# Kernel optimization log

Hardware: AMD Instinct MI355X
Metric: run time of the kernel (lower is better)

## Reference

```python
import jax, jax.numpy as jnp
import numpy as np

B, TQ, TP, D = 4, 512, 512, 256


def setup_inputs() -> dict:
    key = jax.random.key(0)
    ks = jax.random.split(key, 5)
    return {
        "q": jax.random.normal(ks[0], (B, TQ, D), dtype=jnp.float32),
        "p": jax.random.normal(ks[1], (B, TP, D), dtype=jnp.float32),
        "W0": jax.random.normal(ks[2], (D, D), dtype=jnp.float32) / np.sqrt(D),
        "W1": jax.random.normal(ks[3], (D, D), dtype=jnp.float32) / np.sqrt(D),
        "vc": jax.random.normal(ks[4], (D, 1), dtype=jnp.float32) * 0.05,
    }


def reference(q, p, W0, W1, vc):
    # q: [B,Tq,Dq], p: [B,Tp,Dp]
    prod_q = jnp.einsum('bqd,de->bqe', q, W0)   # [B,Tq,dim]
    prod_p = jnp.einsum('bpd,de->bpe', p, W1)   # [B,Tp,dim]
    # additive attention energies: tanh over broadcast sum [B,Tp,Tq,dim]
    energy = jnp.tanh(prod_p[:, :, None, :] + prod_q[:, None, :, :])
    scores = jnp.einsum('bpqe,e->bpq', energy, vc[:, 0])  # [B,Tp,Tq]
    # original softmax is over axis=-2 of [B,Tp,Tq], i.e. the Tp axis
    weights = jax.nn.softmax(scores, axis=1)   # [B,Tp,Tq]
    # weighted sum over the Tq axis of (tiled) q
    attention_q = jnp.einsum('bpq,bqd->bpd', weights, q)  # [B,Tp,Dq]
    return attention_q
```

## Files before the change

### kernel.cpp

```cpp
#include <hip/hip_runtime.h>

#define NB 4
#define TT 512
#define DD 256
#define K2L2E    2.885390081777927f
#define NEG2L2E (-2.885390081777927f)

#if defined(__has_builtin)
# if __has_builtin(__builtin_amdgcn_global_load_lds)
#  define HAS_GLL 1
# endif
#endif

typedef float v2f __attribute__((ext_vector_type(2)));

__device__ __forceinline__ v2f pk_fma(v2f a, v2f b, v2f c) {
#if defined(__has_builtin)
# if __has_builtin(__builtin_elementwise_fma)
    return __builtin_elementwise_fma(a, b, c);
# else
    v2f r; r.x = __builtin_fmaf(a.x, b.x, c.x); r.y = __builtin_fmaf(a.y, b.y, c.y); return r;
# endif
#else
    v2f r; r.x = __builtin_fmaf(a.x, b.x, c.x); r.y = __builtin_fmaf(a.y, b.y, c.y); return r;
#endif
}
__device__ __forceinline__ v2f splat2(float s) { v2f r; r.x = s; r.y = s; return r; }

__device__ __forceinline__ void stage16(const float* __restrict__ g, float* l) {
#ifdef HAS_GLL
    __builtin_amdgcn_global_load_lds((const __attribute__((address_space(1))) void*)g,
                                     (__attribute__((address_space(3))) void*)l, 16, 0, 0);
#else
    *(float4*)l = *(const float4*)g;
#endif
}

__global__ __launch_bounds__(256) void proj_exp_kernel(
    const float* __restrict__ qin, const float* __restrict__ pin,
    const float* __restrict__ W0, const float* __restrict__ W1,
    float* __restrict__ expQ, float* __restrict__ expP)
{
    const int blk = blockIdx.x;
    const int wh = blk >> 8, tid = blk & 255;
    const int m0 = (tid >> 2) * 32, n0 = (tid & 3) * 64;
    const float* A = wh ? pin : qin;
    const float* W = wh ? W1 : W0;
    float* OUT     = wh ? expP : expQ;

    __shared__ __align__(16) float As[32 * 34];
    __shared__ __align__(16) float Bs[32 * 64];

    const int t  = threadIdx.x;
    const int ar = t >> 3, ac4 = (t & 7) * 4;
    const int br = t >> 4, bc4 = (t & 15) * 4;
    const int tn = t >> 4, tm = t & 15;

    const float* Ap = A + (long)(m0 + ar) * DD + ac4;

    float4 av  = *(const float4*)Ap;
    float4 bv0 = *(const float4*)(W + (long)br * DD + n0 + bc4);
    float4 bv1 = *(const float4*)(W + (long)(br + 16) * DD + n0 + bc4);

    float acc[2][4] = {};

    for (int c = 0; c < 8; ++c) {
        As[(ac4 + 0) * 34 + ar] = av.x;
        As[(ac4 + 1) * 34 + ar] = av.y;
        As[(ac4 + 2) * 34 + ar] = av.z;
        As[(ac4 + 3) * 34 + ar] = av.w;
        *(float4*)&Bs[br * 64 + bc4]        = bv0;
        *(float4*)&Bs[(br + 16) * 64 + bc4] = bv1;
        __syncthreads();
        if (c < 7) {
            int k1 = (c + 1) * 32;
            av  = *(const float4*)(Ap + k1);
            bv0 = *(const float4*)(W + (long)(k1 + br) * DD + n0 + bc4);
            bv1 = *(const float4*)(W + (long)(k1 + 16 + br) * DD + n0 + bc4);
        }
        #pragma unroll
        for (int kk = 0; kk < 32; ++kk) {
            float2 a = *(const float2*)&As[kk * 34 + 2 * tm];
            float4 b = *(const float4*)&Bs[kk * 64 + 4 * tn];
            float aa[2] = {a.x, a.y};
            float bb[4] = {b.x, b.y, b.z, b.w};
            #pragma unroll
            for (int i = 0; i < 2; ++i)
                #pragma unroll
                for (int j = 0; j < 4; ++j)
                    acc[i][j] = __builtin_fmaf(aa[i], bb[j], acc[i][j]);
        }
        __syncthreads();
    }

    const int  bi = m0 >> 9;
    const int  ml = (m0 & 511) + 2 * tm;
    #pragma unroll
    for (int j = 0; j < 4; ++j) {
        int d = n0 + 4 * tn + j;
        float2 st;
        st.x = __builtin_amdgcn_exp2f(acc[0][j] * K2L2E);
        st.y = __builtin_amdgcn_exp2f(acc[1][j] * K2L2E);
        *(float2*)(OUT + ((long)bi * DD + d) * TT + ml) = st;
    }
}

__global__ __launch_bounds__(512, 6) void score_kernel(
    const float* __restrict__ expP, const float* __restrict__ expQ,
    const float* __restrict__ vc, float* __restrict__ ebuf, float* __restrict__ lpart)
{
    const int b = blockIdx.z, pt = blockIdx.y, qt = blockIdx.x;
    const int p0 = pt * 32, q0 = qt * 64;
    const int t  = threadIdx.x;
    const int qx = t & 31, py = t >> 5;

    __shared__ __align__(16) float PA[128 * 32];
    __shared__ __align__(16) float QB[128 * 64];
    __shared__ float vcs[DD];

    const float* gP = expP + (long)b * DD * TT + p0;
    const float* gQ = expQ + (long)b * DD * TT + q0;

    #pragma unroll
    for (int s = 0; s < 2; ++s) {
        int f = t + 512 * s, d = f >> 3, off = (f & 7) * 4;
        stage16(gP + (long)d * TT + off, &PA[f * 4]);
    }
    #pragma unroll
    for (int s = 0; s < 4; ++s) {
        int f = t + 512 * s, d = f >> 4, off = (f & 15) * 4;
        stage16(gQ + (long)d * TT + off, &QB[f * 4]);
    }
    if (t < DD) vcs[t] = vc[t];
    __syncthreads();

    v2f acc[2]; acc[0] = splat2(0.f); acc[1] = splat2(0.f);

    for (int c = 0; c < 2; ++c) {
        if (c == 1) {
            __syncthreads();
            #pragma unroll
            for (int s = 0; s < 2; ++s) {
                int f = t + 512 * s, d = f >> 3, off = (f & 7) * 4;
                stage16(gP + (long)(128 + d) * TT + off, &PA[f * 4]);
            }
            #pragma unroll
            for (int s = 0; s < 4; ++s) {
                int f = t + 512 * s, d = f >> 4, off = (f & 15) * 4;
                stage16(gQ + (long)(128 + d) * TT + off, &QB[f * 4]);
            }
            __syncthreads();
        }
        const float* vcb = &vcs[c * 128];
        #pragma unroll 8
        for (int dp = 0; dp < 64; ++dp) {
            float2 vp = *(const float2*)&vcb[2 * dp];
            v2f vsv = splat2(vp.x + vp.y);
            v2f vx  = splat2(vp.x), vy = splat2(vp.y);
            float2 A0 = *(const float2*)&PA[(2 * dp) * 32 + 2 * py];
            float2 A1 = *(const float2*)&PA[(2 * dp + 1) * 32 + 2 * py];
            v2f B0 = *(const v2f*)&QB[(2 * dp) * 64 + 2 * qx];
            v2f B1 = *(const v2f*)&QB[(2 * dp + 1) * 64 + 2 * qx];
            float a0[2] = {A0.x, A0.y}, a1[2] = {A1.x, A1.y};
            #pragma unroll
            for (int i = 0; i < 2; ++i) {
                v2f E0  = splat2(a0[i]) * B0;
                v2f E1  = splat2(a1[i]) * B1;
                v2f u   = (E0 + E1) + 1.0f;
                v2f den = pk_fma(E0, E1, u);
                v2f num = pk_fma(vy, E0, pk_fma(vx, E1, vsv));
                v2f r;
                r.x = __builtin_amdgcn_rcpf(den.x);
                r.y = __builtin_amdgcn_rcpf(den.y);
                acc[i] = pk_fma(num, r, acc[i]);
            }
        }
    }

    float* eb = ebuf + ((long)b * TT + p0) * TT + q0;
    v2f colp = splat2(0.f);
    #pragma unroll
    for (int i = 0; i < 2; ++i) {
        float2 ev;
        ev.x = __builtin_amdgcn_exp2f(acc[i].x * NEG2L2E);
        ev.y = __builtin_amdgcn_exp2f(acc[i].y * NEG2L2E);
        *(float2*)(eb + (long)(2 * py + i) * TT + 2 * qx) = ev;
        colp.x += ev.x; colp.y += ev.y;
    }
    __syncthreads();
    float* scr = (float*)&PA[0];
    *(float2*)&scr[py * 64 + 2 * qx] = make_float2(colp.x, colp.y);
    __syncthreads();
    if (t < 64) {
        float s = 0.f;
        #pragma unroll
        for (int r = 0; r < 16; ++r) s += scr[r * 64 + t];
        lpart[((long)b * 16 + pt) * TT + q0 + t] = s;
    }
}

__global__ __launch_bounds__(128) void out_kernel(
    const float* __restrict__ ebuf, const float* __restrict__ qin,
    const float* __restrict__ lpart, float* __restrict__ out)
{
    const int b = blockIdx.z, pt = blockIdx.y, dt = blockIdx.x;
    const int m0 = pt * 32, n0 = dt * 32;
    const int t  = threadIdx.x;
    const int tm = t >> 4;
    const int tn = t & 15;

    __shared__ __align__(16) float As[64 * 36];
    __shared__ __align__(16) float Bs[64 * 36];
    __shared__ float linv[TT];

    #pragma unroll
    for (int s = 0; s < 4; ++s) {
        int qq = t + 128 * s;
        float sum = 0.f;
        #pragma unroll
        for (int pb = 0; pb < 16; ++pb) sum += lpart[((long)b * 16 + pb) * TT + qq];
        linv[qq] = __builtin_amdgcn_rcpf(sum);
    }
    __syncthreads();

    const float* Ab = ebuf + ((long)b * TT + m0) * TT;
    const float* Bb = qin + (long)b * TT * DD + n0;

    const int ar  = t >> 2;
    const int akc = (t & 3) * 4;
    const int brr = t >> 3;
    const int bc4 = (t & 7) * 4;

    float4 av[4], bv[4];
    #pragma unroll
    for (int u = 0; u < 4; ++u) {
        av[u] = *(const float4*)(Ab + (long)ar * TT + 16 * u + akc);
        bv[u] = *(const float4*)(Bb + (long)(brr + 16 * u) * DD + bc4);
    }

    v2f acc[4]; acc[0] = splat2(0.f); acc[1] = splat2(0.f);
    acc[2] = splat2(0.f); acc[3] = splat2(0.f);

    for (int c = 0; c < 8; ++c) {
        const int k0 = c * 64;
        #pragma unroll
        for (int u = 0; u < 4; ++u) {
            int kl = 16 * u + akc;
            As[(kl + 0) * 36 + ar] = av[u].x;
            As[(kl + 1) * 36 + ar] = av[u].y;
            As[(kl + 2) * 36 + ar] = av[u].z;
            As[(kl + 3) * 36 + ar] = av[u].w;
            float s = linv[k0 + brr + 16 * u];
            float4 w;
            w.x = bv[u].x * s; w.y = bv[u].y * s; w.z = bv[u].z * s; w.w = bv[u].w * s;
            *(float4*)&Bs[(brr + 16 * u) * 36 + bc4] = w;
        }
        __syncthreads();
        if (c < 7) {
            int k1 = (c + 1) * 64;
            #pragma unroll
            for (int u = 0; u < 4; ++u) {
                av[u] = *(const float4*)(Ab + (long)ar * TT + k1 + 16 * u + akc);
                bv[u] = *(const float4*)(Bb + (long)(k1 + brr + 16 * u) * DD + bc4);
            }
        }
        #pragma unroll
        for (int kk = 0; kk < 64; ++kk) {
            float4 a = *(const float4*)&As[kk * 36 + 4 * tm];
            v2f bb = *(const v2f*)&Bs[kk * 36 + 2 * tn];
            acc[0] = pk_fma(splat2(a.x), bb, acc[0]);
            acc[1] = pk_fma(splat2(a.y), bb, acc[1]);
            acc[2] = pk_fma(splat2(a.z), bb, acc[2]);
            acc[3] = pk_fma(splat2(a.w), bb, acc[3]);
        }
        __syncthreads();
    }

    #pragma unroll
    for (int i = 0; i < 4; ++i) {
        *(float2*)(out + ((long)b * TT + m0 + 4 * tm + i) * DD + n0 + 2 * tn) =
            make_float2(acc[i].x, acc[i].y);
    }
}

extern "C" void kernel_launch(void* const* d_in, const int* in_sizes, int n_in,
                              void* d_out, int out_size, void* d_ws, size_t ws_size,
                              hipStream_t stream) {
    const float* q  = (const float*)d_in[0];
    const float* p  = (const float*)d_in[1];
    const float* W0 = (const float*)d_in[2];
    const float* W1 = (const float*)d_in[3];
    const float* vc = (const float*)d_in[4];
    float* out = (float*)d_out;

    float* ws    = (float*)d_ws;
    float* expQ  = ws;
    float* expP  = ws + 524288;
    float* ebuf  = ws + 1048576;
    float* lpart = ws + 2097152;

    proj_exp_kernel<<<dim3(512), 256, 0, stream>>>(q, p, W0, W1, expQ, expP);
    score_kernel<<<dim3(8, 16, NB), 512, 0, stream>>>(expP, expQ, vc, ebuf, lpart);
    out_kernel<<<dim3(8, 16, NB), 128, 0, stream>>>(ebuf, q, lpart, out);
}
```

Baseline: 124.4 us.

## Combine four dims per reciprocal in score loop, transpose expP, split-K out kernel

The score kernel now merges four tanh terms into one rational expression, so it needs one reciprocal per four dimensions instead of per two, which cuts transcendental throughput pressure. To support float4 reads along d, expP is stored p-major and the projection kernel writes it with float4 stores. The output kernel moves to 256 threads with a four-wave split-K over each 64-wide chunk, stages q directly into LDS, folds the softmax normaliser into A, and reduces the partial sums in shared memory. Products of four (1+E) terms can overflow or lose precision for large projections, and the out kernel loses its register prefetch.

Result: no change. 123.8 us (-0.5%).

```diff
diff --git a/kernel.cpp b/kernel.cpp
--- a/kernel.cpp
+++ b/kernel.cpp
@@ -46,7 +46,6 @@
     const int m0 = (tid >> 2) * 32, n0 = (tid & 3) * 64;
     const float* A = wh ? pin : qin;
     const float* W = wh ? W1 : W0;
-    float* OUT     = wh ? expP : expQ;
 
     __shared__ __align__(16) float As[32 * 34];
     __shared__ __align__(16) float Bs[32 * 64];
@@ -54,7 +53,8 @@
     const int t  = threadIdx.x;
     const int ar = t >> 3, ac4 = (t & 7) * 4;
     const int br = t >> 4, bc4 = (t & 15) * 4;
-    const int tn = t >> 4, tm = t & 15;
+    const int tm = wh ? (t >> 4) : (t & 15);
+    const int tn = wh ? (t & 15) : (t >> 4);
 
     const float* Ap = A + (long)(m0 + ar) * DD + ac4;
 
@@ -93,15 +93,27 @@
         __syncthreads();
     }
 
-    const int  bi = m0 >> 9;
-    const int  ml = (m0 & 511) + 2 * tm;
-    #pragma unroll
-    for (int j = 0; j < 4; ++j) {
-        int d = n0 + 4 * tn + j;
-        float2 st;
-        st.x = __builtin_amdgcn_exp2f(acc[0][j] * K2L2E);
-        st.y = __builtin_amdgcn_exp2f(acc[1][j] * K2L2E);
-        *(float2*)(OUT + ((long)bi * DD + d) * TT + ml) = st;
+    const int bi = m0 >> 9;
+    const int ml = m0 & 511;
+    if (wh) {
+        #pragma unroll
+        for (int i = 0; i < 2; ++i) {
+            float4 st;
+            st.x = __builtin_amdgcn_exp2f(acc[i][0] * K2L2E);
+            st.y = __builtin_amdgcn_exp2f(acc[i][1] * K2L2E);
+            st.z = __builtin_amdgcn_exp2f(acc[i][2] * K2L2E);
+            st.w = __builtin_amdgcn_exp2f(acc[i][3] * K2L2E);
+            *(float4*)(expP + ((long)bi * TT + ml + 2 * tm + i) * DD + n0 + 4 * tn) = st;
+        }
+    } else {
+        #pragma unroll
+        for (int j = 0; j < 4; ++j) {
+            int d = n0 + 4 * tn + j;
+            float2 st;
+            st.x = __builtin_amdgcn_exp2f(acc[0][j] * K2L2E);
+            st.y = __builtin_amdgcn_exp2f(acc[1][j] * K2L2E);
+            *(float2*)(expQ + ((long)bi * DD + d) * TT + ml + 2 * tm) = st;
+        }
     }
 }
 
@@ -114,22 +126,22 @@
     const int t  = threadIdx.x;
     const int qx = t & 31, py = t >> 5;
 
-    __shared__ __align__(16) float PA[128 * 32];
+    __shared__ __align__(16) float PA[32 * 128];
     __shared__ __align__(16) float QB[128 * 64];
-    __shared__ float vcs[DD];
-
-    const float* gP = expP + (long)b * DD * TT + p0;
+    __shared__ __align__(16) float vcs[DD];
+
+    const float* gP = expP + ((long)b * TT + p0) * DD;
     const float* gQ = expQ + (long)b * DD * TT + q0;
 
     #pragma unroll
     for (int s = 0; s < 2; ++s) {
-        int f = t + 512 * s, d = f >> 3, off = (f & 7) * 4;
-        stage16(gP + (long)d * TT + off, &PA[f * 4]);
+        int f = t + 512 * s, pr = f >> 5, d4 = (f & 31) * 4;
+        stage16(gP + (long)pr * DD + d4, &PA[f * 4]);
     }
     #pragma unroll
     for (int s = 0; s < 4; ++s) {
-        int f = t + 512 * s, d = f >> 4, off = (f & 15) * 4;
-        stage16(gQ + (long)d * TT + off, &QB[f * 4]);
+        int f = t + 512 * s, d = f >> 4, o4 = (f & 15) * 4;
+        stage16(gQ + (long)d * TT + o4, &QB[f * 4]);
     }
     if (t < DD) vcs[t] = vc[t];
     __syncthreads();
@@ -141,34 +153,40 @@
             __syncthreads();
             #pragma unroll
             for (int s = 0; s < 2; ++s) {
-                int f = t + 512 * s, d = f >> 3, off = (f & 7) * 4;
-                stage16(gP + (long)(128 + d) * TT + off, &PA[f * 4]);
+                int f = t + 512 * s, pr = f >> 5, d4 = (f & 31) * 4;
+                stage16(gP + (long)pr * DD + 128 + d4, &PA[f * 4]);
             }
             #pragma unroll
             for (int s = 0; s < 4; ++s) {
-                int f = t + 512 * s, d = f >> 4, off = (f & 15) * 4;
-                stage16(gQ + (long)(128 + d) * TT + off, &QB[f * 4]);
+                int f = t + 512 * s, d = f >> 4, o4 = (f & 15) * 4;
+                stage16(gQ + (long)(128 + d) * TT + o4, &QB[f * 4]);
             }
             __syncthreads();
         }
         const float* vcb = &vcs[c * 128];
-        #pragma unroll 8
-        for (int dp = 0; dp < 64; ++dp) {
-            float2 vp = *(const float2*)&vcb[2 * dp];
-            v2f vsv = splat2(vp.x + vp.y);
-            v2f vx  = splat2(vp.x), vy = splat2(vp.y);
-            float2 A0 = *(const float2*)&PA[(2 * dp) * 32 + 2 * py];
-            float2 A1 = *(const float2*)&PA[(2 * dp + 1) * 32 + 2 * py];
-            v2f B0 = *(const v2f*)&QB[(2 * dp) * 64 + 2 * qx];
-            v2f B1 = *(const v2f*)&QB[(2 * dp + 1) * 64 + 2 * qx];
-            float a0[2] = {A0.x, A0.y}, a1[2] = {A1.x, A1.y};
+        #pragma unroll 4
+        for (int dq = 0; dq < 32; ++dq) {
+            float4 vq = *(const float4*)&vcb[4 * dq];
+            float vs01 = vq.x + vq.y, vs23 = vq.z + vq.w;
+            float4 aq0 = *(const float4*)&PA[(2 * py) * 128 + 4 * dq];
+            float4 aq1 = *(const float4*)&PA[(2 * py + 1) * 128 + 4 * dq];
+            v2f B0 = *(const v2f*)&QB[(4 * dq + 0) * 64 + 2 * qx];
+            v2f B1 = *(const v2f*)&QB[(4 * dq + 1) * 64 + 2 * qx];
+            v2f B2 = *(const v2f*)&QB[(4 * dq + 2) * 64 + 2 * qx];
+            v2f B3 = *(const v2f*)&QB[(4 * dq + 3) * 64 + 2 * qx];
             #pragma unroll
             for (int i = 0; i < 2; ++i) {
-                v2f E0  = splat2(a0[i]) * B0;
-                v2f E1  = splat2(a1[i]) * B1;
-                v2f u   = (E0 + E1) + 1.0f;
-                v2f den = pk_fma(E0, E1, u);
-                v2f num = pk_fma(vy, E0, pk_fma(vx, E1, vsv));
+                float4 a = i ? aq1 : aq0;
+                v2f E0 = splat2(a.x) * B0;
+                v2f E1 = splat2(a.y) * B1;
+                v2f E2 = splat2(a.z) * B2;
+                v2f E3 = splat2(a.w) * B3;
+                v2f t01 = pk_fma(E0, E1, (E0 + E1) + 1.0f);
+                v2f t23 = pk_fma(E2, E3, (E2 + E3) + 1.0f);
+                v2f den = t01 * t23;
+                v2f n01 = pk_fma(splat2(vq.x), E1, pk_fma(splat2(vq.y), E0, splat2(vs01)));
+                v2f n23 = pk_fma(splat2(vq.z), E3, pk_fma(splat2(vq.w), E2, splat2(vs23)));
+                v2f num = pk_fma(n01, t23, n23 * t01);
                 v2f r;
                 r.x = __builtin_amdgcn_rcpf(den.x);
                 r.y = __builtin_amdgcn_rcpf(den.y);
@@ -199,23 +217,26 @@
     }
 }
 
-__global__ __launch_bounds__(128) void out_kernel(
+__global__ __launch_bounds__(256) void out_kernel(
     const float* __restrict__ ebuf, const float* __restrict__ qin,
     const float* __restrict__ lpart, float* __restrict__ out)
 {
     const int b = blockIdx.z, pt = blockIdx.y, dt = blockIdx.x;
     const int m0 = pt * 32, n0 = dt * 32;
-    const int t  = threadIdx.x;
-    const int tm = t >> 4;
-    const int tn = t & 15;
-
-    __shared__ __align__(16) float As[64 * 36];
-    __shared__ __align__(16) float Bs[64 * 36];
+    const int t    = threadIdx.x;
+    const int wv   = t >> 6;
+    const int lane = t & 63;
+    const int pg   = lane >> 3;
+    const int dg   = lane & 7;
+
+    __shared__ __align__(16) float smem[4 * 32 * 36];
     __shared__ float linv[TT];
-
-    #pragma unroll
-    for (int s = 0; s < 4; ++s) {
-        int qq = t + 128 * s;
+    float* As = smem;
+    float* Bs = smem + 64 * 36;
+
+    #pragma unroll
+    for (int s = 0; s < 2; ++s) {
+        int qq = t + 256 * s;
         float sum = 0.f;
         #pragma unroll
         for (int pb = 0; pb < 16; ++pb) sum += lpart[((long)b * 16 + pb) * TT + qq];
@@ -226,60 +247,68 @@
     const float* Ab = ebuf + ((long)b * TT + m0) * TT;
     const float* Bb = qin + (long)b * TT * DD + n0;
 
-    const int ar  = t >> 2;
-    const int akc = (t & 3) * 4;
-    const int brr = t >> 3;
-    const int bc4 = (t & 7) * 4;
-
-    float4 av[4], bv[4];
-    #pragma unroll
-    for (int u = 0; u < 4; ++u) {
-        av[u] = *(const float4*)(Ab + (long)ar * TT + 16 * u + akc);
-        bv[u] = *(const float4*)(Bb + (long)(brr + 16 * u) * DD + bc4);
-    }
-
-    v2f acc[4]; acc[0] = splat2(0.f); acc[1] = splat2(0.f);
-    acc[2] = splat2(0.f); acc[3] = splat2(0.f);
+    const int ar = t >> 3, ak4 = (t & 7) * 4;
+
+    v2f acc[4][2];
+    #pragma unroll
+    for (int i = 0; i < 4; ++i) { acc[i][0] = splat2(0.f); acc[i][1] = splat2(0.f); }
 
     for (int c = 0; c < 8; ++c) {
         const int k0 = c * 64;
         #pragma unroll
-        for (int u = 0; u < 4; ++u) {
-            int kl = 16 * u + akc;
-            As[(kl + 0) * 36 + ar] = av[u].x;
-            As[(kl + 1) * 36 + ar] = av[u].y;
-            As[(kl + 2) * 36 + ar] = av[u].z;
-            As[(kl + 3) * 36 + ar] = av[u].w;
-            float s = linv[k0 + brr + 16 * u];
-            float4 w;
-            w.x = bv[u].x * s; w.y = bv[u].y * s; w.z = bv[u].z * s; w.w = bv[u].w * s;
-            *(float4*)&Bs[(brr + 16 * u) * 36 + bc4] = w;
+        for (int s = 0; s < 2; ++s) {
+            int f = t + 256 * s, kr = f >> 3, d4 = (f & 7) * 4;
+            stage16(Bb + (long)(k0 + kr) * DD + d4, &Bs[f * 4]);
+        }
+        #pragma unroll
+        for (int s = 0; s < 2; ++s) {
+            int kq = ak4 + 32 * s;
+            float4 a = *(const float4*)(Ab + (long)ar * TT + k0 + kq);
+            float4 lv = *(const float4*)&linv[k0 + kq];
+            As[(kq + 0) * 36 + ar] = a.x * lv.x;
+            As[(kq + 1) * 36 + ar] = a.y * lv.y;
+            As[(kq + 2) * 36 + ar] = a.z * lv.z;
+            As[(kq + 3) * 36 + ar] = a.w * lv.w;
         }
         __syncthreads();
-        if (c < 7) {
-            int k1 = (c + 1) * 64;
-            #pragma unroll
-            for (int u = 0; u < 4; ++u) {
-                av[u] = *(const float4*)(Ab + (long)ar * TT + k1 + 16 * u + akc);
-                bv[u] = *(const float4*)(Bb + (long)(k1 + brr + 16 * u) * DD + bc4);
-            }
-        }
-        #pragma unroll
-        for (int kk = 0; kk < 64; ++kk) {
-            float4 a = *(const float4*)&As[kk * 36 + 4 * tm];
-            v2f bb = *(const v2f*)&Bs[kk * 36 + 2 * tn];
-            acc[0] = pk_fma(splat2(a.x), bb, acc[0]);
-            acc[1] = pk_fma(splat2(a.y), bb, acc[1]);
-            acc[2] = pk_fma(splat2(a.z), bb, acc[2]);
-            acc[3] = pk_fma(splat2(a.w), bb, acc[3]);
+        const int kb = 16 * wv;
+        #pragma unroll
+        for (int u = 0; u < 16; ++u) {
+            int kk = kb + u;
+            float4 a = *(const float4*)&As[kk * 36 + 4 * pg];
+            v2f b0 = *(const v2f*)&Bs[kk * 32 + 4 * dg];
+            v2f b1 = *(const v2f*)&Bs[kk * 32 + 4 * dg + 2];
+            acc[0][0] = pk_fma(splat2(a.x), b0, acc[0][0]);
+            acc[0][1] = pk_fma(splat2(a.x), b1, acc[0][1]);
+            acc[1][0] = pk_fma(splat2(a.y), b0, acc[1][0]);
+            acc[1][1] = pk_fma(splat2(a.y), b1, acc[1][1]);
+            acc[2][0] = pk_fma(splat2(a.z), b0, acc[2][0]);
+            acc[2][1] = pk_fma(splat2(a.z), b1, acc[2][1]);
+            acc[3][0] = pk_fma(splat2(a.w), b0, acc[3][0]);
+            acc[3][1] = pk_fma(splat2(a.w), b1, acc[3][1]);
         }
         __syncthreads();
     }
 
+    float* scr = smem;
     #pragma unroll
     for (int i = 0; i < 4; ++i) {
-        *(float2*)(out + ((long)b * TT + m0 + 4 * tm + i) * DD + n0 + 2 * tn) =
-            make_float2(acc[i].x, acc[i].y);
+        *(v2f*)&scr[wv * 1152 + (4 * pg + i) * 36 + 4 * dg]     = acc[i][0];
+        *(v2f*)&scr[wv * 1152 + (4 * pg + i) * 36 + 4 * dg + 2] = acc[i][1];
+    }
+    __syncthreads();
+    {
+        int pr = t >> 3, d0 = (t & 7) * 4;
+        float4 s0 = *(const float4*)&scr[0 * 1152 + pr * 36 + d0];
+        float4 s1 = *(const float4*)&scr[1 * 1152 + pr * 36 + d0];
+        float4 s2 = *(const float4*)&scr[2 * 1152 + pr * 36 + d0];
+        float4 s3 = *(const float4*)&scr[3 * 1152 + pr * 36 + d0];
+        float4 v;
+        v.x = (s0.x + s1.x) + (s2.x + s3.x);
+        v.y = (s0.y + s1.y) + (s2.y + s3.y);
+        v.z = (s0.z + s1.z) + (s2.z + s3.z);
+        v.w = (s0.w + s1.w) + (s2.w + s3.w);
+        *(float4*)(out + ((long)b * TT + m0 + pr) * DD + n0 + d0) = v;
     }
 }
 
@@ -301,5 +330,5 @@
 
     proj_exp_kernel<<<dim3(512), 256, 0, stream>>>(q, p, W0, W1, expQ, expP);
     score_kernel<<<dim3(8, 16, NB), 512, 0, stream>>>(expP, expQ, vc, ebuf, lpart);
-    out_kernel<<<dim3(8, 16, NB), 128, 0, stream>>>(ebuf, q, lpart, out);
-}
+    out_kernel<<<dim3(8, 16, NB), 256, 0, stream>>>(ebuf, q, lpart, out);
+}
```
